# Kernel tuning notes

Hardware: AMD Instinct MI355X
Metric: run time of the kernel (lower is better)

## Reference

```python
import jax, jax.numpy as jnp
import numpy as np

HALFKP = 64 * 5 * 64          # 20480
PAD = HALFKP                  # padding row index
L1, L2, L3 = 256, 31, 32
NB = 8                        # layer-stack / psqt buckets
EMB_DIM = L1 + NB             # 264


def setup_inputs() -> dict:
    key = jax.random.key(0)
    ks = jax.random.split(key, 16)
    B = 16384
    w_idx = jax.random.randint(ks[0], (B, 32), 0, HALFKP + 1)
    b_idx = jax.random.randint(ks[1], (B, 32), 0, HALFKP + 1)
    us = jax.random.uniform(ks[2], (B,), dtype=jnp.float32)
    them = jax.random.uniform(ks[3], (B,), dtype=jnp.float32)
    piece_count = jax.random.randint(ks[4], (B,), 2, 33)
    sigma = 0.025
    emb = jax.random.uniform(ks[5], (HALFKP + 1, EMB_DIM), jnp.float32, -sigma, sigma)
    emb = emb.at[PAD].set(0.0)
    def lin(k, out_f, in_f):
        bound = 1.0 / np.sqrt(in_f)
        k1, k2 = jax.random.split(k)
        W = jax.random.uniform(k1, (out_f, in_f), jnp.float32, -bound, bound)
        b = jax.random.uniform(k2, (out_f,), jnp.float32, -bound, bound)
        return W, b
    # StackedLinear init: replicate slot-0 weights across all buckets
    w1_0, b1_0 = lin(ks[6], L2 + 1, L1)
    w1 = jnp.tile(w1_0, (NB, 1)); b1 = jnp.tile(b1_0, NB)
    fw1 = jnp.zeros((L2 + 1, L1), jnp.float32)
    fb1 = jnp.zeros((L2 + 1,), jnp.float32)
    w2_0, b2_0 = lin(ks[7], L3, L2 * 2)
    w2 = jnp.tile(w2_0, (NB, 1)); b2 = jnp.tile(b2_0, NB)
    wo_0, _ = lin(ks[8], 1, L3)
    wo = jnp.tile(wo_0, (NB, 1)); bo = jnp.zeros((NB,), jnp.float32)
    return {"emb": emb, "w1": w1, "b1": b1, "fw1": fw1, "fb1": fb1,
            "w2": w2, "b2": b2, "wo": wo, "bo": bo,
            "us": us, "them": them,
            "w_idx": w_idx, "b_idx": b_idx, "piece_count": piece_count}


def reference(emb, w1, b1, fw1, fb1, w2, b2, wo, bo, us, them,
              w_idx, b_idx, piece_count):
    emb_eff = emb.at[PAD].set(0.0)                      # padding row contributes 0
    wp = emb_eff[w_idx].sum(axis=1)                     # [B, 264]
    bp = emb_eff[b_idx].sum(axis=1)
    w, wpsqt = wp[:, :L1], wp[:, L1:]
    b, bpsqt = bp[:, :L1], bp[:, L1:]
    us_c = us[:, None]; them_c = them[:, None]
    l0 = us_c * jnp.concatenate([w, b], 1) + them_c * jnp.concatenate([b, w], 1)
    l0 = jnp.clip(l0, 0.0, 1.0)                         # [B, 512]
    h = L1 // 2
    l0 = jnp.concatenate([l0[:, :h] * l0[:, h:2*h],
                          l0[:, 2*h:3*h] * l0[:, 3*h:]], 1) * (127.0 / 128.0)  # [B,256]
    bucket = jnp.clip((piece_count - 1) // 4, 0, 7)     # [B]
    # l1: factorized stacked linear, gather the bucket's slice only
    W1 = (w1 + jnp.tile(fw1, (NB, 1))).reshape(NB, L2 + 1, L1)
    B1 = (b1 + jnp.tile(fb1, NB)).reshape(NB, L2 + 1)
    l1c = jnp.einsum('bi,bji->bj', l0, W1[bucket]) + B1[bucket]   # [B,32]
    l1x, l1x_out = l1c[:, :L2], l1c[:, L2:]
    l1x = jnp.clip(jnp.concatenate([l1x * l1x * (255.0 / 256.0), l1x], 1), 0.0, 1.0)  # [B,62]
    W2 = w2.reshape(NB, L3, L2 * 2)
    l2x = jnp.clip(jnp.einsum('bi,bji->bj', l1x, W2[bucket]) + b2.reshape(NB, L3)[bucket], 0.0, 1.0)
    Wo = wo.reshape(NB, 1, L3)
    l3c = jnp.einsum('bi,bji->bj', l2x, Wo[bucket]) + bo.reshape(NB, 1)[bucket]       # [B,1]
    fc_out = l3c + l1x_out
    bk = bucket[:, None]
    psqt_out = (jnp.take_along_axis(wpsqt, bk, 1) - jnp.take_along_axis(bpsqt, bk, 1)) * (us_c - 0.5)
    return fc_out + psqt_out                            # [B,1]
```

## Files before the change

### kernel.cpp

```cpp
#include <hip/hip_runtime.h>

#define EMBD 264
#define NROWS 20481
#define NR4   5121
#define QS 5080.0f
#define INVQS (1.0f/5080.0f)

typedef short short8 __attribute__((ext_vector_type(8)));
typedef float f32x4  __attribute__((ext_vector_type(4)));
typedef unsigned u32x4 __attribute__((ext_vector_type(4)));

__device__ __forceinline__ float clamp01(float x) { return fminf(fmaxf(x, 0.f), 1.f); }
__device__ __forceinline__ unsigned short f2bf(float f) {
    unsigned u = __float_as_uint(f);
    u += 0x7fffu + ((u >> 16) & 1u);
    return (unsigned short)(u >> 16);
}

__global__ void prep_all(const float* __restrict__ emb, unsigned int* __restrict__ emb8,
                         float* __restrict__ psqt,
                         const float* __restrict__ w1, const float* __restrict__ fw1,
                         const float* __restrict__ b1, const float* __restrict__ fb1,
                         const float* __restrict__ w2,
                         unsigned short* __restrict__ w1b, float* __restrict__ b1c,
                         float* __restrict__ w2p) {
    if (blockIdx.x < NR4) {
        const int r = blockIdx.x * 4 + (threadIdx.x >> 6);
        const int t = threadIdx.x & 63;
        if (r >= NROWS) return;
        const bool pad = (r == NROWS - 1);
        const float2 va = *(const float2*)(emb + (size_t)r * EMBD + 2 * t);
        const float2 vb = *(const float2*)(emb + (size_t)r * EMBD + 128 + 2 * t);
        int q0 = pad ? 128 : (int)rintf(va.x * QS) + 128;
        int q1 = pad ? 128 : (int)rintf(vb.x * QS) + 128;
        int q2 = pad ? 128 : (int)rintf(va.y * QS) + 128;
        int q3 = pad ? 128 : (int)rintf(vb.y * QS) + 128;
        q0 = min(max(q0, 0), 255); q1 = min(max(q1, 0), 255);
        q2 = min(max(q2, 0), 255); q3 = min(max(q3, 0), 255);
        emb8[(size_t)r * 64 + t] = (unsigned)q0 | ((unsigned)q1 << 8) |
                                   ((unsigned)q2 << 16) | ((unsigned)q3 << 24);
        if (t < 8) {
            float pv = emb[(size_t)r * EMBD + 256 + t];
            psqt[r * 8 + t] = pad ? 0.f : pv;
        }
    } else {
        const int e = (blockIdx.x - NR4) * 256 + threadIdx.x;
        const int bkt = e >> 13, rem = e & 8191;
        const int s = rem >> 10, rem2 = rem & 1023;
        const int nt = rem2 >> 9, rem3 = rem2 & 511;
        const int ln = rem3 >> 3, j = rem3 & 7;
        const int n  = nt * 16 + (ln & 15);
        const int hi = ln >> 4;
        const int k  = s * 32 + hi * 8 + j;
        const float v = w1[(bkt * 32 + n) * 256 + k] + fw1[n * 256 + k];
        w1b[e] = f2bf(v);
        if (e < 256) b1c[e] = b1[e] + fb1[e & 31];
        if (e < 16384) {
            const int jr = e >> 6, i = e & 63;
            float x = 0.f;
            if (i < 31) x = w2[jr * 62 + i];
            else if (i >= 32 && i < 63) x = w2[jr * 62 + i - 1];
            w2p[e] = x;
        }
    }
}

__global__ __launch_bounds__(256, 8) void g_phase1p(
    const unsigned int* __restrict__ emb8,
    const float* __restrict__ psqt,
    const float* __restrict__ us,
    const float* __restrict__ them,
    const int*   __restrict__ w_idx,
    const int*   __restrict__ b_idx,
    const int*   __restrict__ pcnt,
    unsigned short* __restrict__ Ag,
    float* __restrict__ psq_g,
    int B)
{
    const int bid   = blockIdx.x;
    const int tile  = bid & 1;
    const int chunk = bid >> 1;
    const int lane  = threadIdx.x & 63;
    const int wv    = threadIdx.x >> 6;
    const int slot  = lane >> 3;
    const int pos   = lane & 7;
    const unsigned off = (unsigned)(tile * 128 + pos * 16);
    const unsigned M = 0x00FF00FFu;
    const float c127 = 127.f / 128.f;

    for (int rr = 0; rr < 4; ++rr) {
        const int grow = __builtin_amdgcn_readfirstlane(chunk * 16 + wv * 4 + rr);
        const float usv = us[grow];
        const float thv = them[grow];

        const int iv = (lane < 32) ? w_idx[grow * 32 + lane]
                                   : b_idx[grow * 32 + (lane - 32)];

        float ps = 0.f;
        if (tile == 0) {
            int bucket = (pcnt[grow] - 1) >> 2;
            bucket = bucket > 7 ? 7 : bucket;
            bucket = __builtin_amdgcn_readfirstlane(bucket);
            ps = psqt[(size_t)iv * 8 + bucket];
        }

        uint4 vw[4], vb4[4];
#pragma unroll
        for (int k = 0; k < 4; ++k) {
            const int r = __shfl(iv, k * 8 + slot);
            vw[k] = *(const uint4*)((const char*)emb8 + (((unsigned)r << 8) + off));
        }
#pragma unroll
        for (int k = 0; k < 4; ++k) {
            const int r = __shfl(iv, 32 + k * 8 + slot);
            vb4[k] = *(const uint4*)((const char*)emb8 + (((unsigned)r << 8) + off));
        }

        unsigned a0w[4] = {0,0,0,0}, a1w[4] = {0,0,0,0};
        unsigned a0b[4] = {0,0,0,0}, a1b[4] = {0,0,0,0};
#pragma unroll
        for (int k = 0; k < 4; ++k) {
            a0w[0] += vw[k].x & M;  a1w[0] += (vw[k].x >> 8) & M;
            a0w[1] += vw[k].y & M;  a1w[1] += (vw[k].y >> 8) & M;
            a0w[2] += vw[k].z & M;  a1w[2] += (vw[k].z >> 8) & M;
            a0w[3] += vw[k].w & M;  a1w[3] += (vw[k].w >> 8) & M;
            a0b[0] += vb4[k].x & M; a1b[0] += (vb4[k].x >> 8) & M;
            a0b[1] += vb4[k].y & M; a1b[1] += (vb4[k].y >> 8) & M;
            a0b[2] += vb4[k].z & M; a1b[2] += (vb4[k].z >> 8) & M;
            a0b[3] += vb4[k].w & M; a1b[3] += (vb4[k].w >> 8) & M;
        }

#pragma unroll
        for (int q = 0; q < 4; ++q) {
            a0w[q] += __shfl_xor(a0w[q], 8);  a0w[q] += __shfl_xor(a0w[q], 16);  a0w[q] += __shfl_xor(a0w[q], 32);
            a1w[q] += __shfl_xor(a1w[q], 8);  a1w[q] += __shfl_xor(a1w[q], 16);  a1w[q] += __shfl_xor(a1w[q], 32);
            a0b[q] += __shfl_xor(a0b[q], 8);  a0b[q] += __shfl_xor(a0b[q], 16);  a0b[q] += __shfl_xor(a0b[q], 32);
            a1b[q] += __shfl_xor(a1b[q], 8);  a1b[q] += __shfl_xor(a1b[q], 16);  a1b[q] += __shfl_xor(a1b[q], 32);
        }

        if (tile == 0) {
            ps += __shfl_xor(ps, 16);
            ps += __shfl_xor(ps, 8);
            ps += __shfl_xor(ps, 4);
            ps += __shfl_xor(ps, 2);
            ps += __shfl_xor(ps, 1);
            const float psq_w = __shfl(ps, 0);
            const float psq_b = __shfl(ps, 32);
            if (lane == 0) psq_g[grow] = (psq_w - psq_b) * (usv - 0.5f);
        }

        unsigned wlo[4], whi[4];
#pragma unroll
        for (int q = 0; q < 4; ++q) {
            float op[2], oq[2];
#pragma unroll
            for (int h = 0; h < 2; ++h) {
                const int sh = h << 4;
                const float wj  = ((int)((a0w[q] >> sh) & 0xffffu) - 4096) * INVQS;
                const float bj  = ((int)((a0b[q] >> sh) & 0xffffu) - 4096) * INVQS;
                const float wj1 = ((int)((a1w[q] >> sh) & 0xffffu) - 4096) * INVQS;
                const float bj1 = ((int)((a1b[q] >> sh) & 0xffffu) - 4096) * INVQS;
                const float P0 = clamp01(usv * wj  + thv * bj);
                const float P1 = clamp01(usv * wj1 + thv * bj1);
                const float Q0 = clamp01(usv * bj  + thv * wj);
                const float Q1 = clamp01(usv * bj1 + thv * wj1);
                op[h] = P0 * P1 * c127;
                oq[h] = Q0 * Q1 * c127;
            }
            wlo[q] = (unsigned)f2bf(op[0]) | ((unsigned)f2bf(op[1]) << 16);
            whi[q] = (unsigned)f2bf(oq[0]) | ((unsigned)f2bf(oq[1]) << 16);
        }
        if (slot == 0) {
            unsigned short* d1 = Ag + (size_t)grow * 256 + tile * 64 + pos * 8;
            u32x4 v1 = { wlo[0], wlo[1], wlo[2], wlo[3] };
            u32x4 v2 = { whi[0], whi[1], whi[2], whi[3] };
            __builtin_nontemporal_store(v1, (u32x4*)d1);
            __builtin_nontemporal_store(v2, (u32x4*)(d1 + 128));
        }
    }
}

__global__ __launch_bounds__(512) void g_phase23(
    const unsigned short* __restrict__ Ag,
    const float* __restrict__ psq_g,
    const unsigned short* __restrict__ w1b,
    const float* __restrict__ b1c,
    const float* __restrict__ w2p,
    const float* __restrict__ b2,
    const float* __restrict__ wo,
    const float* __restrict__ bo,
    const int*   __restrict__ pcnt,
    float* __restrict__ out,
    int B)
{
    __shared__ unsigned short A_lds[16 * 280];
    __shared__ float l1c[8 * 16 * 36];
    __shared__ float psq_lds[16];
    __shared__ int   bkt_lds[16];

    const int tid  = threadIdx.x;
    const int lane = tid & 63;
    const int w    = tid >> 6;

    {
        const int m = tid >> 5, c = tid & 31;
        *(uint4*)&A_lds[m * 280 + c * 8] =
            *(const uint4*)(Ag + ((size_t)blockIdx.x * 16 + m) * 256 + c * 8);
    }
    if (tid < 16) {
        const int row = blockIdx.x * 16 + tid;
        int bucket = (pcnt[row] - 1) >> 2;
        bkt_lds[tid] = bucket > 7 ? 7 : bucket;
        psq_lds[tid] = psq_g[row];
    }
    __syncthreads();

    {
        const int col = lane & 15;
        const int hi  = lane >> 4;
        const int bkt = w;
        f32x4 acc[2];
        acc[0] = (f32x4){0.f, 0.f, 0.f, 0.f};
        acc[1] = (f32x4){0.f, 0.f, 0.f, 0.f};

#pragma unroll
        for (int s = 0; s < 8; ++s) {
            const short8 a = *((const short8*)&A_lds[col * 280 + s * 32 + hi * 8]);
#pragma unroll
            for (int nt = 0; nt < 2; ++nt) {
                const short8 bf = *((const short8*)&w1b[(((bkt * 8 + s) * 2 + nt) * 64 + lane) * 8]);
                acc[nt] = __builtin_amdgcn_mfma_f32_16x16x32_bf16(a, bf, acc[nt], 0, 0, 0);
            }
        }
#pragma unroll
        for (int nt = 0; nt < 2; ++nt) {
            const float bias = b1c[bkt * 32 + nt * 16 + col];
#pragma unroll
            for (int reg = 0; reg < 4; ++reg) {
                const int mr = hi * 4 + reg;
                l1c[(bkt * 16 + mr) * 36 + nt * 16 + col] = acc[nt][reg] + bias;
            }
        }
    }
    __syncthreads();

    if (tid < 256) {
        const int row = tid >> 4;
        const int jj  = tid & 15;
        const int bkt = bkt_lds[row];
        const float4* crow = (const float4*)&l1c[(bkt * 16 + row) * 36];
        float4 c4[8];
#pragma unroll
        for (int b5 = 0; b5 < 8; ++b5) c4[b5] = crow[b5];

        const float4* wr0 = (const float4*)&w2p[(bkt * 32 + jj) * 64];
        const float4* wr1 = (const float4*)&w2p[(bkt * 32 + jj + 16) * 64];
        float acc0 = 0.f, acc1 = 0.f;
        const float kq = 255.f / 256.f;
#pragma unroll
        for (int b5 = 0; b5 < 8; ++b5) {
            const float4 cv = c4[b5];
            float4 sq, ln;
            sq.x = clamp01(cv.x * cv.x * kq); ln.x = clamp01(cv.x);
            sq.y = clamp01(cv.y * cv.y * kq); ln.y = clamp01(cv.y);
            sq.z = clamp01(cv.z * cv.z * kq); ln.z = clamp01(cv.z);
            sq.w = clamp01(cv.w * cv.w * kq); ln.w = clamp01(cv.w);
            const float4 ws0 = wr0[b5], wl0 = wr0[8 + b5];
            const float4 ws1 = wr1[b5], wl1 = wr1[8 + b5];
            acc0 += sq.x * ws0.x + sq.y * ws0.y + sq.z * ws0.z + sq.w * ws0.w;
            acc0 += ln.x * wl0.x + ln.y * wl0.y + ln.z * wl0.z + ln.w * wl0.w;
            acc1 += sq.x * ws1.x + sq.y * ws1.y + sq.z * ws1.z + sq.w * ws1.w;
            acc1 += ln.x * wl1.x + ln.y * wl1.y + ln.z * wl1.z + ln.w * wl1.w;
        }
        const float t0 = clamp01(acc0 + b2[bkt * 32 + jj])      * wo[bkt * 32 + jj];
        const float t1 = clamp01(acc1 + b2[bkt * 32 + jj + 16]) * wo[bkt * 32 + jj + 16];
        float tsum = t0 + t1;
        tsum += __shfl_xor(tsum, 8);
        tsum += __shfl_xor(tsum, 4);
        tsum += __shfl_xor(tsum, 2);
        tsum += __shfl_xor(tsum, 1);
        if (jj == 0) {
            out[blockIdx.x * 16 + row] = tsum + bo[bkt] + c4[7].w + psq_lds[row];
        }
    }
}

__global__ __launch_bounds__(256) void nnue_fwd_f32(
    const float* __restrict__ emb,
    const float* __restrict__ w1e, const float* __restrict__ fw1,
    const float* __restrict__ b1e, const float* __restrict__ fb1,
    const float* __restrict__ w2,  const float* __restrict__ b2,
    const float* __restrict__ wo,  const float* __restrict__ bo,
    const float* __restrict__ us,  const float* __restrict__ them,
    const int* __restrict__ w_idx, const int* __restrict__ b_idx,
    const int* __restrict__ pcnt,  float* __restrict__ out, int B)
{
    const int lane = threadIdx.x & 63;
    const int row  = blockIdx.x * 4 + (threadIdx.x >> 6);
    if (row >= B) return;
    const float usv = us[row];
    const float thv = them[row];
    int bucket = (pcnt[row] - 1) >> 2;
    bucket = bucket > 7 ? 7 : bucket;
    bucket = __builtin_amdgcn_readfirstlane(bucket);
    const int kk = lane & 31;
    const int myidx = (lane < 32) ? w_idx[row * 32 + kk] : b_idx[row * 32 + kk];
    float ps = emb[(size_t)myidx * EMBD + 256 + bucket];
    ps += __shfl_xor(ps, 16); ps += __shfl_xor(ps, 8);
    ps += __shfl_xor(ps, 4);  ps += __shfl_xor(ps, 2); ps += __shfl_xor(ps, 1);
    const float psq_w = __shfl(ps, 0);
    const float psq_b = __shfl(ps, 32);
    float4 aw = make_float4(0,0,0,0), ab = make_float4(0,0,0,0);
#pragma unroll
    for (int k = 0; k < 32; ++k) {
        const int iw = __shfl(myidx, k);
        const int ib = __shfl(myidx, 32 + k);
        const float4 vw = *((const float4*)(emb + (size_t)iw * EMBD) + lane);
        const float4 vb = *((const float4*)(emb + (size_t)ib * EMBD) + lane);
        aw.x += vw.x; aw.y += vw.y; aw.z += vw.z; aw.w += vw.w;
        ab.x += vb.x; ab.y += vb.y; ab.z += vb.z; ab.w += vb.w;
    }
    float4 p, q;
    p.x = clamp01(usv*aw.x + thv*ab.x); p.y = clamp01(usv*aw.y + thv*ab.y);
    p.z = clamp01(usv*aw.z + thv*ab.z); p.w = clamp01(usv*aw.w + thv*ab.w);
    q.x = clamp01(usv*ab.x + thv*aw.x); q.y = clamp01(usv*ab.y + thv*aw.y);
    q.z = clamp01(usv*ab.z + thv*aw.z); q.w = clamp01(usv*ab.w + thv*aw.w);
    float4 po, qo;
    po.x = __shfl_xor(p.x,32); po.y = __shfl_xor(p.y,32);
    po.z = __shfl_xor(p.z,32); po.w = __shfl_xor(p.w,32);
    qo.x = __shfl_xor(q.x,32); qo.y = __shfl_xor(q.y,32);
    qo.z = __shfl_xor(q.z,32); qo.w = __shfl_xor(q.w,32);
    const float c127 = 127.f/128.f;
    float4 l0f;
    if (lane < 32) { l0f.x=p.x*po.x*c127; l0f.y=p.y*po.y*c127; l0f.z=p.z*po.z*c127; l0f.w=p.w*po.w*c127; }
    else           { l0f.x=q.x*qo.x*c127; l0f.y=q.y*qo.y*c127; l0f.z=q.z*qo.z*c127; l0f.w=q.w*qo.w*c127; }
    float part[32];
    const float4* w1p = (const float4*)(w1e + (size_t)bucket * 8192);
    const float4* f1p = (const float4*)fw1;
#pragma unroll
    for (int j = 0; j < 32; ++j) {
        float4 wv = w1p[j*64 + lane];
        float4 fv = f1p[j*64 + lane];
        wv.x+=fv.x; wv.y+=fv.y; wv.z+=fv.z; wv.w+=fv.w;
        part[j] = l0f.x*wv.x + l0f.y*wv.y + l0f.z*wv.z + l0f.w*wv.w;
    }
#pragma unroll
    for (int j = 0; j < 32; ++j) {
        float v = part[j];
        v += __shfl_xor(v,32); v += __shfl_xor(v,16); v += __shfl_xor(v,8);
        v += __shfl_xor(v,4);  v += __shfl_xor(v,2);  v += __shfl_xor(v,1);
        part[j] = v + b1e[bucket*32 + j] + fb1[j];
    }
    const float l1x_out = part[31];
    float acc2 = 0.f;
    if (lane < 32) {
        const float* w2r = w2 + (size_t)(bucket*32 + lane) * 62;
#pragma unroll
        for (int i = 0; i < 31; ++i) {
            const float a = part[i];
            acc2 += clamp01(a*a*(255.f/256.f)) * w2r[i];
            acc2 += clamp01(a) * w2r[31+i];
        }
        acc2 += b2[bucket*32 + lane];
        acc2 = clamp01(acc2) * wo[bucket*32 + lane];
    }
    acc2 += __shfl_xor(acc2,16); acc2 += __shfl_xor(acc2,8);
    acc2 += __shfl_xor(acc2,4);  acc2 += __shfl_xor(acc2,2); acc2 += __shfl_xor(acc2,1);
    if (lane == 0)
        out[row] = acc2 + bo[bucket] + l1x_out + (psq_w - psq_b) * (usv - 0.5f);
}

extern "C" void kernel_launch(void* const* d_in, const int* in_sizes, int n_in,
                              void* d_out, int out_size, void* d_ws, size_t ws_size,
                              hipStream_t stream) {
    const float* emb  = (const float*)d_in[0];
    const float* w1   = (const float*)d_in[1];
    const float* b1   = (const float*)d_in[2];
    const float* fw1  = (const float*)d_in[3];
    const float* fb1  = (const float*)d_in[4];
    const float* w2   = (const float*)d_in[5];
    const float* b2   = (const float*)d_in[6];
    const float* wo   = (const float*)d_in[7];
    const float* bo   = (const float*)d_in[8];
    const float* us   = (const float*)d_in[9];
    const float* them = (const float*)d_in[10];
    const int*   wi   = (const int*)d_in[11];
    const int*   bi   = (const int*)d_in[12];
    const int*   pc   = (const int*)d_in[13];
    float* out = (float*)d_out;

    const int B = in_sizes[9];

    const size_t emb8_bytes = (size_t)NROWS * 256;
    const size_t psqt_bytes = (size_t)NROWS * 8 * 4;
    const size_t w1b_bytes  = 65536 * 2;
    const size_t b1c_bytes  = 256 * 4;
    const size_t w2p_bytes  = 16384 * 4;
    const size_t Ag_bytes   = (size_t)B * 256 * 2;
    const size_t psq_bytes  = (size_t)B * 4;
    const size_t need = emb8_bytes + psqt_bytes + w1b_bytes + b1c_bytes +
                        w2p_bytes + Ag_bytes + psq_bytes;

    if (ws_size >= need && (B % 16) == 0) {
        char* p = (char*)d_ws;
        unsigned int*   emb8 = (unsigned int*)p;     p += emb8_bytes;
        float*          psqt = (float*)p;            p += psqt_bytes;
        unsigned short* w1b  = (unsigned short*)p;   p += w1b_bytes;
        float*          b1c  = (float*)p;            p += b1c_bytes;
        float*          w2p  = (float*)p;            p += w2p_bytes;
        unsigned short* Ag   = (unsigned short*)p;   p += Ag_bytes;
        float*          psq  = (float*)p;

        prep_all<<<NR4 + 256, 256, 0, stream>>>(emb, emb8, psqt,
                                                w1, fw1, b1, fb1, w2, w1b, b1c, w2p);
        g_phase1p<<<(B / 16) * 2, 256, 0, stream>>>(emb8, psqt, us, them, wi, bi, pc,
                                                    Ag, psq, B);
        g_phase23<<<B / 16, 512, 0, stream>>>(Ag, psq, w1b, b1c, w2p,
                                              b2, wo, bo, pc, out, B);
    } else {
        nnue_fwd_f32<<<(B + 3) / 4, 256, 0, stream>>>(emb, w1, fw1, b1, fb1,
                                                      w2, b2, wo, bo, us, them, wi, bi, pc, out, B);
    }
}
```

Measured before the change: 151.5 us.

## Stage feature-column slices of quantized embedding table in LDS for gather-sum

Phase 1 is restructured so each 1024-thread block loads one 8-feature column slice of the entire 8-bit embedding table (160 KB) into LDS. Each thread then accumulates one batch row by gathering from LDS instead of issuing scattered global loads. Indices are pre-packed to 16 bits in the prep kernel, the W1 bf16 layout is permuted to match the new feature-slot ordering, and the A matrix is written in a group-major layout that phase 2/3 reads. This trades global gather traffic for a large LDS footprint (one block per CU), redundant table loads across 256 blocks, and hardcodes B==16384.

Result: slower. 170.6 us (+12.6%).

```diff
diff --git a/kernel.cpp b/kernel.cpp
--- a/kernel.cpp
+++ b/kernel.cpp
@@ -8,7 +8,6 @@
 
 typedef short short8 __attribute__((ext_vector_type(8)));
 typedef float f32x4  __attribute__((ext_vector_type(4)));
-typedef unsigned u32x4 __attribute__((ext_vector_type(4)));
 
 __device__ __forceinline__ float clamp01(float x) { return fminf(fmaxf(x, 0.f), 1.f); }
 __device__ __forceinline__ unsigned short f2bf(float f) {
@@ -17,13 +16,19 @@
     return (unsigned short)(u >> 16);
 }
 
+__device__ __forceinline__ int slot2feat(int c) {
+    const int g = c >> 3, e = c & 7;
+    return (e < 4) ? (g * 4 + e) : (128 + g * 4 + (e - 4));
+}
+
 __global__ void prep_all(const float* __restrict__ emb, unsigned int* __restrict__ emb8,
                          float* __restrict__ psqt,
                          const float* __restrict__ w1, const float* __restrict__ fw1,
                          const float* __restrict__ b1, const float* __restrict__ fb1,
                          const float* __restrict__ w2,
+                         const int* __restrict__ w_idx, const int* __restrict__ b_idx,
                          unsigned short* __restrict__ w1b, float* __restrict__ b1c,
-                         float* __restrict__ w2p) {
+                         float* __restrict__ w2p, unsigned* __restrict__ ids32) {
     if (blockIdx.x < NR4) {
         const int r = blockIdx.x * 4 + (threadIdx.x >> 6);
         const int t = threadIdx.x & 63;
@@ -43,7 +48,7 @@
             float pv = emb[(size_t)r * EMBD + 256 + t];
             psqt[r * 8 + t] = pad ? 0.f : pv;
         }
-    } else {
+    } else if (blockIdx.x < NR4 + 256) {
         const int e = (blockIdx.x - NR4) * 256 + threadIdx.x;
         const int bkt = e >> 13, rem = e & 8191;
         const int s = rem >> 10, rem2 = rem & 1023;
@@ -51,7 +56,8 @@
         const int ln = rem3 >> 3, j = rem3 & 7;
         const int n  = nt * 16 + (ln & 15);
         const int hi = ln >> 4;
-        const int k  = s * 32 + hi * 8 + j;
+        const int kslot = s * 32 + hi * 8 + j;
+        const int k = slot2feat(kslot);
         const float v = w1[(bkt * 32 + n) * 256 + k] + fw1[n * 256 + k];
         w1b[e] = f2bf(v);
         if (e < 256) b1c[e] = b1[e] + fb1[e & 31];
@@ -62,121 +68,138 @@
             else if (i >= 32 && i < 63) x = w2[jr * 62 + i - 1];
             w2p[e] = x;
         }
-    }
-}
-
-__global__ __launch_bounds__(256, 8) void g_phase1p(
+    } else {
+        const int bi = blockIdx.x - (NR4 + 256);
+        const int d0 = (bi * 256 + threadIdx.x) * 4;
+#pragma unroll
+        for (int u = 0; u < 4; ++u) {
+            const int d = d0 + u;
+            const int row = d >> 5;
+            const int kp = (d & 31) << 1;
+            const int a = (kp < 32) ? w_idx[row * 32 + kp]     : b_idx[row * 32 + kp - 32];
+            const int b = (kp < 32) ? w_idx[row * 32 + kp + 1] : b_idx[row * 32 + kp - 31];
+            ids32[d] = ((unsigned)a & 0xffffu) | ((unsigned)b << 16);
+        }
+    }
+}
+
+__global__ __launch_bounds__(1024) void g_phase1L(
     const unsigned int* __restrict__ emb8,
     const float* __restrict__ psqt,
+    const unsigned short* __restrict__ ids16,
     const float* __restrict__ us,
     const float* __restrict__ them,
-    const int*   __restrict__ w_idx,
-    const int*   __restrict__ b_idx,
     const int*   __restrict__ pcnt,
     unsigned short* __restrict__ Ag,
     float* __restrict__ psq_g,
     int B)
 {
-    const int bid   = blockIdx.x;
-    const int tile  = bid & 1;
-    const int chunk = bid >> 1;
-    const int lane  = threadIdx.x & 63;
-    const int wv    = threadIdx.x >> 6;
-    const int slot  = lane >> 3;
-    const int pos   = lane & 7;
-    const unsigned off = (unsigned)(tile * 128 + pos * 16);
-    const unsigned M = 0x00FF00FFu;
-    const float c127 = 127.f / 128.f;
-
-    for (int rr = 0; rr < 4; ++rr) {
-        const int grow = __builtin_amdgcn_readfirstlane(chunk * 16 + wv * 4 + rr);
-        const float usv = us[grow];
-        const float thv = them[grow];
-
-        const int iv = (lane < 32) ? w_idx[grow * 32 + lane]
-                                   : b_idx[grow * 32 + (lane - 32)];
-
-        float ps = 0.f;
-        if (tile == 0) {
-            int bucket = (pcnt[grow] - 1) >> 2;
+    __shared__ unsigned long long ldsT[20480];
+
+    const int g    = blockIdx.x & 31;
+    const int jb   = blockIdx.x >> 5;
+    const int tid  = threadIdx.x;
+    const int lane = tid & 63;
+    const int wv   = tid >> 6;
+    const int SL   = B >> 3;
+
+    {
+        const int chunk = SL >> 5;
+        const int pw    = chunk >> 4;
+        const int prow0 = jb * SL + g * chunk + wv * pw;
+        for (int rr = 0; rr < pw; ++rr) {
+            const int prow = prow0 + rr;
+            const float usv = us[prow];
+            int bucket = (pcnt[prow] - 1) >> 2;
             bucket = bucket > 7 ? 7 : bucket;
-            bucket = __builtin_amdgcn_readfirstlane(bucket);
-            ps = psqt[(size_t)iv * 8 + bucket];
-        }
-
-        uint4 vw[4], vb4[4];
-#pragma unroll
-        for (int k = 0; k < 4; ++k) {
-            const int r = __shfl(iv, k * 8 + slot);
-            vw[k] = *(const uint4*)((const char*)emb8 + (((unsigned)r << 8) + off));
-        }
-#pragma unroll
-        for (int k = 0; k < 4; ++k) {
-            const int r = __shfl(iv, 32 + k * 8 + slot);
-            vb4[k] = *(const uint4*)((const char*)emb8 + (((unsigned)r << 8) + off));
-        }
-
-        unsigned a0w[4] = {0,0,0,0}, a1w[4] = {0,0,0,0};
-        unsigned a0b[4] = {0,0,0,0}, a1b[4] = {0,0,0,0};
-#pragma unroll
-        for (int k = 0; k < 4; ++k) {
-            a0w[0] += vw[k].x & M;  a1w[0] += (vw[k].x >> 8) & M;
-            a0w[1] += vw[k].y & M;  a1w[1] += (vw[k].y >> 8) & M;
-            a0w[2] += vw[k].z & M;  a1w[2] += (vw[k].z >> 8) & M;
-            a0w[3] += vw[k].w & M;  a1w[3] += (vw[k].w >> 8) & M;
-            a0b[0] += vb4[k].x & M; a1b[0] += (vb4[k].x >> 8) & M;
-            a0b[1] += vb4[k].y & M; a1b[1] += (vb4[k].y >> 8) & M;
-            a0b[2] += vb4[k].z & M; a1b[2] += (vb4[k].z >> 8) & M;
-            a0b[3] += vb4[k].w & M; a1b[3] += (vb4[k].w >> 8) & M;
-        }
-
-#pragma unroll
-        for (int q = 0; q < 4; ++q) {
-            a0w[q] += __shfl_xor(a0w[q], 8);  a0w[q] += __shfl_xor(a0w[q], 16);  a0w[q] += __shfl_xor(a0w[q], 32);
-            a1w[q] += __shfl_xor(a1w[q], 8);  a1w[q] += __shfl_xor(a1w[q], 16);  a1w[q] += __shfl_xor(a1w[q], 32);
-            a0b[q] += __shfl_xor(a0b[q], 8);  a0b[q] += __shfl_xor(a0b[q], 16);  a0b[q] += __shfl_xor(a0b[q], 32);
-            a1b[q] += __shfl_xor(a1b[q], 8);  a1b[q] += __shfl_xor(a1b[q], 16);  a1b[q] += __shfl_xor(a1b[q], 32);
-        }
-
-        if (tile == 0) {
+            const unsigned pidx = ids16[(size_t)prow * 64 + lane];
+            float ps = psqt[(size_t)pidx * 8 + bucket];
             ps += __shfl_xor(ps, 16);
             ps += __shfl_xor(ps, 8);
             ps += __shfl_xor(ps, 4);
             ps += __shfl_xor(ps, 2);
             ps += __shfl_xor(ps, 1);
-            const float psq_w = __shfl(ps, 0);
-            const float psq_b = __shfl(ps, 32);
-            if (lane == 0) psq_g[grow] = (psq_w - psq_b) * (usv - 0.5f);
-        }
-
-        unsigned wlo[4], whi[4];
-#pragma unroll
-        for (int q = 0; q < 4; ++q) {
-            float op[2], oq[2];
+            const float pw_ = __shfl(ps, 0);
+            const float pb_ = __shfl(ps, 32);
+            if (lane == 0) psq_g[prow] = (pw_ - pb_) * (usv - 0.5f);
+        }
+    }
+
+#pragma unroll
+    for (int c = 0; c < 20; ++c) {
+        const int r = c * 1024 + tid;
+        ldsT[r] = *(const unsigned long long*)(emb8 + (size_t)r * 64 + 2 * g);
+    }
+    __syncthreads();
+
+    const unsigned M = 0x00FF00FFu;
+    const float c127 = 127.f / 128.f;
+    const int passes = SL >> 10;
+    for (int p = 0; p < passes; ++p) {
+        const int row = jb * SL + wv * (SL >> 4) + p * 64 + lane;
+        const float usv = us[row];
+        const float thv = them[row];
+        const unsigned short* idr = ids16 + (size_t)row * 64;
+
+        unsigned awlo0 = 0, awlo1 = 0, awhi0 = 0, awhi1 = 0;
+        unsigned ablo0 = 0, ablo1 = 0, abhi0 = 0, abhi1 = 0;
+#pragma unroll 8
+        for (int k = 0; k < 32; k += 2) {
+            const unsigned pr = *(const unsigned*)(idr + k);
+            const unsigned i0 = pr & 0xffffu, i1 = pr >> 16;
+            unsigned long long v0 = ldsT[i0 < 20480u ? i0 : 0u];
+            unsigned long long v1 = ldsT[i1 < 20480u ? i1 : 0u];
+            if (i0 == 20480u) v0 = 0x8080808080808080ULL;
+            if (i1 == 20480u) v1 = 0x8080808080808080ULL;
+            const unsigned a0 = (unsigned)v0, a1 = (unsigned)(v0 >> 32);
+            const unsigned b0 = (unsigned)v1, b1 = (unsigned)(v1 >> 32);
+            awlo0 += a0 & M;  awhi0 += (a0 >> 8) & M;
+            awlo1 += a1 & M;  awhi1 += (a1 >> 8) & M;
+            awlo0 += b0 & M;  awhi0 += (b0 >> 8) & M;
+            awlo1 += b1 & M;  awhi1 += (b1 >> 8) & M;
+        }
+#pragma unroll 8
+        for (int k = 32; k < 64; k += 2) {
+            const unsigned pr = *(const unsigned*)(idr + k);
+            const unsigned i0 = pr & 0xffffu, i1 = pr >> 16;
+            unsigned long long v0 = ldsT[i0 < 20480u ? i0 : 0u];
+            unsigned long long v1 = ldsT[i1 < 20480u ? i1 : 0u];
+            if (i0 == 20480u) v0 = 0x8080808080808080ULL;
+            if (i1 == 20480u) v1 = 0x8080808080808080ULL;
+            const unsigned a0 = (unsigned)v0, a1 = (unsigned)(v0 >> 32);
+            const unsigned b0 = (unsigned)v1, b1 = (unsigned)(v1 >> 32);
+            ablo0 += a0 & M;  abhi0 += (a0 >> 8) & M;
+            ablo1 += a1 & M;  abhi1 += (a1 >> 8) & M;
+            ablo0 += b0 & M;  abhi0 += (b0 >> 8) & M;
+            ablo1 += b1 & M;  abhi1 += (b1 >> 8) & M;
+        }
+
+        float P[4], Q[4];
+        const unsigned slo[2] = { awlo0, awlo1 }, shi[2] = { awhi0, awhi1 };
+        const unsigned tlo[2] = { ablo0, ablo1 }, thi[2] = { abhi0, abhi1 };
+#pragma unroll
+        for (int d = 0; d < 2; ++d) {
 #pragma unroll
             for (int h = 0; h < 2; ++h) {
                 const int sh = h << 4;
-                const float wj  = ((int)((a0w[q] >> sh) & 0xffffu) - 4096) * INVQS;
-                const float bj  = ((int)((a0b[q] >> sh) & 0xffffu) - 4096) * INVQS;
-                const float wj1 = ((int)((a1w[q] >> sh) & 0xffffu) - 4096) * INVQS;
-                const float bj1 = ((int)((a1b[q] >> sh) & 0xffffu) - 4096) * INVQS;
-                const float P0 = clamp01(usv * wj  + thv * bj);
-                const float P1 = clamp01(usv * wj1 + thv * bj1);
-                const float Q0 = clamp01(usv * bj  + thv * wj);
-                const float Q1 = clamp01(usv * bj1 + thv * wj1);
-                op[h] = P0 * P1 * c127;
-                oq[h] = Q0 * Q1 * c127;
+                const float wA = ((int)((slo[d] >> sh) & 0xffffu) - 4096) * INVQS;
+                const float wB = ((int)((shi[d] >> sh) & 0xffffu) - 4096) * INVQS;
+                const float bA = ((int)((tlo[d] >> sh) & 0xffffu) - 4096) * INVQS;
+                const float bB = ((int)((thi[d] >> sh) & 0xffffu) - 4096) * INVQS;
+                const float PA = clamp01(usv * wA + thv * bA);
+                const float PB = clamp01(usv * wB + thv * bB);
+                const float QA = clamp01(usv * bA + thv * wA);
+                const float QB = clamp01(usv * bB + thv * wB);
+                P[2 * d + h] = PA * PB * c127;
+                Q[2 * d + h] = QA * QB * c127;
             }
-            wlo[q] = (unsigned)f2bf(op[0]) | ((unsigned)f2bf(op[1]) << 16);
-            whi[q] = (unsigned)f2bf(oq[0]) | ((unsigned)f2bf(oq[1]) << 16);
-        }
-        if (slot == 0) {
-            unsigned short* d1 = Ag + (size_t)grow * 256 + tile * 64 + pos * 8;
-            u32x4 v1 = { wlo[0], wlo[1], wlo[2], wlo[3] };
-            u32x4 v2 = { whi[0], whi[1], whi[2], whi[3] };
-            __builtin_nontemporal_store(v1, (u32x4*)d1);
-            __builtin_nontemporal_store(v2, (u32x4*)(d1 + 128));
-        }
+        }
+        uint4 o;
+        o.x = (unsigned)f2bf(P[0]) | ((unsigned)f2bf(P[1]) << 16);
+        o.y = (unsigned)f2bf(P[2]) | ((unsigned)f2bf(P[3]) << 16);
+        o.z = (unsigned)f2bf(Q[0]) | ((unsigned)f2bf(Q[1]) << 16);
+        o.w = (unsigned)f2bf(Q[2]) | ((unsigned)f2bf(Q[3]) << 16);
+        *(uint4*)(Ag + ((size_t)g * B + row) * 8) = o;
     }
 }
 
@@ -203,9 +226,9 @@
     const int w    = tid >> 6;
 
     {
-        const int m = tid >> 5, c = tid & 31;
-        *(uint4*)&A_lds[m * 280 + c * 8] =
-            *(const uint4*)(Ag + ((size_t)blockIdx.x * 16 + m) * 256 + c * 8);
+        const int gg = tid >> 4, m = tid & 15;
+        *(uint4*)&A_lds[m * 280 + gg * 8] =
+            *(const uint4*)(Ag + ((size_t)gg * B + blockIdx.x * 16 + m) * 8);
     }
     if (tid < 16) {
         const int row = blockIdx.x * 16 + tid;
@@ -398,10 +421,11 @@
     const size_t w2p_bytes  = 16384 * 4;
     const size_t Ag_bytes   = (size_t)B * 256 * 2;
     const size_t psq_bytes  = (size_t)B * 4;
+    const size_t ids_bytes  = (size_t)B * 64 * 2;
     const size_t need = emb8_bytes + psqt_bytes + w1b_bytes + b1c_bytes +
-                        w2p_bytes + Ag_bytes + psq_bytes;
-
-    if (ws_size >= need && (B % 16) == 0) {
+                        w2p_bytes + Ag_bytes + psq_bytes + ids_bytes;
+
+    if (ws_size >= need && B == 16384) {
         char* p = (char*)d_ws;
         unsigned int*   emb8 = (unsigned int*)p;     p += emb8_bytes;
         float*          psqt = (float*)p;            p += psqt_bytes;
@@ -409,12 +433,14 @@
         float*          b1c  = (float*)p;            p += b1c_bytes;
         float*          w2p  = (float*)p;            p += w2p_bytes;
         unsigned short* Ag   = (unsigned short*)p;   p += Ag_bytes;
-        float*          psq  = (float*)p;
-
-        prep_all<<<NR4 + 256, 256, 0, stream>>>(emb, emb8, psqt,
-                                                w1, fw1, b1, fb1, w2, w1b, b1c, w2p);
-        g_phase1p<<<(B / 16) * 2, 256, 0, stream>>>(emb8, psqt, us, them, wi, bi, pc,
-                                                    Ag, psq, B);
+        float*          psq  = (float*)p;            p += psq_bytes;
+        unsigned*       ids  = (unsigned*)p;
+
+        prep_all<<<NR4 + 256 + 512, 256, 0, stream>>>(emb, emb8, psqt,
+                                                      w1, fw1, b1, fb1, w2,
+                                                      wi, bi, w1b, b1c, w2p, ids);
+        g_phase1L<<<256, 1024, 0, stream>>>(emb8, psqt, (const unsigned short*)ids,
+                                            us, them, pc, Ag, psq, B);
         g_phase23<<<B / 16, 512, 0, stream>>>(Ag, psq, w1b, b1c, w2p,
                                               b2, wo, bo, pc, out, B);
     } else {
```
